# Kernel tuning notes

Hardware: AMD Instinct MI355X
Metric: run time of the kernel (lower is better)

The kernel has to match this reference:

```python
import jax, jax.numpy as jnp
import numpy as np
import math

EMBED = 256
HEADS = 8
HD = EMBED // HEADS  # 32
NB = 3               # n_behaviors
C = NB * NB + 1      # 10 behavior-pair classes
NUM_BUCKETS = 32
MAX_DIST = 40
EPS = 1e-12
B, L = 4, 512


def _rel_bucket(seq_len, num_buckets=NUM_BUCKETS, max_distance=MAX_DIST):
    """T5-style relative position buckets, matching RelativePositionBias._relative_position_bucket."""
    pos = jnp.arange(seq_len)
    relative_position = pos[None, :] - pos[:, None]  # k - q
    n = -relative_position
    nb = num_buckets // 2
    ret = (n < 0).astype(jnp.int32) * nb
    n = jnp.abs(n)
    max_exact = nb // 2
    is_small = n < max_exact
    nf = jnp.maximum(n, 1).astype(jnp.float32)  # clamp to avoid log(0); masked by is_small anyway
    val_large = max_exact + (jnp.log(nf / max_exact) / math.log(max_distance / max_exact) * (nb - max_exact)).astype(jnp.int32)
    val_large = jnp.minimum(val_large, nb - 1)
    return ret + jnp.where(is_small, n, val_large)


def setup_inputs() -> dict:
    key = jax.random.key(0)
    ks = jax.random.split(key, 12)
    s = 0.02
    return {
        "input_tensor": jax.random.normal(ks[0], (B, L, EMBED), jnp.float32),
        "attention_mask": jnp.zeros((B, 1, L, L), jnp.float32),
        "type_seq": jax.random.randint(ks[1], (B, L), 0, NB + 1),
        "Wq": jax.random.normal(ks[2], (NB + 1, EMBED, HEADS, HD), jnp.float32) * s,
        "Wk": jax.random.normal(ks[3], (NB + 1, EMBED, HEADS, HD), jnp.float32) * s,
        "Wv": jax.random.normal(ks[4], (NB + 1, EMBED, HEADS, HD), jnp.float32) * s,
        "W1": jax.random.normal(ks[5], (NB, HEADS, HD, HD), jnp.float32) * s,
        "alpha1": jax.random.normal(ks[6], (C, NB, HEADS), jnp.float32),
        "W2": jax.random.normal(ks[7], (NB, HEADS, HD, HD), jnp.float32) * s,
        "alpha2": jax.random.normal(ks[8], (C, NB, HEADS), jnp.float32),
        "rp_tables": jax.random.normal(ks[9], (C, NUM_BUCKETS, HEADS), jnp.float32) * s,
        "ln_gamma": jnp.ones((EMBED,), jnp.float32),
        "ln_beta": jnp.zeros((EMBED,), jnp.float32),
    }


def reference(input_tensor, attention_mask, type_seq, Wq, Wk, Wv, W1, alpha1, W2, alpha2, rp_tables, ln_gamma, ln_beta):
    bsz, seq_len, emb = input_tensor.shape
    ts = type_seq
    # behavior pair matrix: 0 if either side is padding, else (tq-1)*NB + tk in [1, NB^2]
    bm = ((ts[:, :, None] * ts[:, None, :]) != 0).astype(jnp.int32)
    bm = bm * ((ts[:, :, None] - 1) * NB + ts[:, None, :])  # [B,L,L]

    # --- relative position bias, gathered per behavior pair ---
    bucket = _rel_bucket(seq_len)                 # [L,L]
    vals = rp_tables[:, bucket, :]                # [C,L,L,H]
    qi = jnp.arange(seq_len)[None, :, None]
    ki = jnp.arange(seq_len)[None, None, :]
    bias = vals[bm, qi, ki]                       # [B,L,L,H] gathered along C per pair
    bias = jnp.transpose(bias, (0, 3, 1, 2))      # [B,H,L,L]

    # --- behavior-gated QKV ---
    oh = jax.nn.one_hot(ts, NB + 1, dtype=input_tensor.dtype)  # [B,L,NB+1]
    q = jnp.einsum('BLH,bHhd,BLb->BhLd', input_tensor, Wq, oh)
    k = jnp.einsum('BLH,bHhd,BLb->BhLd', input_tensor, Wk, oh)
    v = jnp.einsum('BLH,bHhd,BLb->BhLd', input_tensor, Wv, oh)

    # --- bilinear scores with per-pair mixing matrices ---
    W1_ = jnp.einsum('bhmn,Cbh->Chmn', W1, jax.nn.softmax(alpha1, axis=1))
    att_all = jnp.einsum('BhQm,Chmn,BhKn->BhQKC', q, W1_, k)  # [B,H,L,L,C]
    scores = jnp.take_along_axis(att_all, bm[:, None, :, :, None], axis=4)[..., 0]
    scores = scores * (1.0 / math.sqrt(HD)) + bias + attention_mask
    probs = jax.nn.softmax(scores, axis=-1)  # dropout=0.0 -> identity

    # --- behavior-mixed value aggregation ---
    W2_ = jnp.einsum('bhmn,Cbh->Chmn', W2, jax.nn.softmax(alpha2, axis=1))
    oh_bm = jax.nn.one_hot(bm, C, dtype=probs.dtype)          # [B,L,L,C]
    pC = probs[:, :, :, :, None] * oh_bm[:, None]             # [B,H,L,L,C]
    ctx = jnp.einsum('BhQKC,Chnm,BhKn->BhQm', pC, W2_, v)     # [B,H,L,d]

    ctx = jnp.transpose(ctx, (0, 2, 1, 3)).reshape(bsz, seq_len, emb)
    x = ctx + input_tensor  # out_dropout=0.0
    mu = jnp.mean(x, axis=-1, keepdims=True)
    var = jnp.mean(jnp.square(x - mu), axis=-1, keepdims=True)
    return (x - mu) / jnp.sqrt(var + EPS) * ln_gamma + ln_beta
```

## Files before the change

### kernel.cpp

```cpp
#include <hip/hip_runtime.h>
#include <math.h>

#define BB 4
#define LL 512
#define EMB 256
#define NH 8
#define HD 32
#define NB_ 3
#define CCN 10
#define NBKT 32
#define SCALE 0.17677669529663687f

typedef __bf16 bf16_t;
typedef __attribute__((ext_vector_type(8))) bf16_t bf16x8;
typedef __attribute__((ext_vector_type(4))) float f32x4;

__device__ __forceinline__ unsigned short f2b(float f) {
    unsigned int u = __float_as_uint(f);
    u += 0x7FFF + ((u >> 16) & 1);
    return (unsigned short)(u >> 16);
}
__device__ __forceinline__ float b2f(unsigned short s) {
    return __uint_as_float(((unsigned int)s) << 16);
}
__device__ __forceinline__ unsigned pack2(float a, float b) {
    return (unsigned)f2b(a) | ((unsigned)f2b(b) << 16);
}
__device__ __forceinline__ int bm_of(int tq, int tk) {
    return (tq * tk != 0) ? ((tq - 1) * 3 + tk) : 0;
}
__device__ __forceinline__ unsigned long long shfl_up64(unsigned long long v, int d) {
    unsigned lo = (unsigned)__shfl_up((int)(unsigned)v, d, 64);
    unsigned hi = (unsigned)__shfl_up((int)(v >> 32), d, 64);
    return (((unsigned long long)hi) << 32) | lo;
}

__device__ __forceinline__ void sort512(const int* __restrict__ tsb, int* spk,
                                        unsigned long long* wtll, int* msc, int tid) {
    int ty0 = tsb[2 * tid], ty1 = tsb[2 * tid + 1];
    unsigned long long pk = (1ULL << (16 * ty0)) + (1ULL << (16 * ty1));
    unsigned long long v = pk;
    int lane = tid & 63;
#pragma unroll
    for (int off = 1; off < 64; off <<= 1) {
        unsigned long long o = shfl_up64(v, off);
        if (lane >= off) v += o;
    }
    int w = tid >> 6;
    if (lane == 63) wtll[w] = v;
    __syncthreads();
    unsigned long long pre = 0, tot = 0;
#pragma unroll
    for (int i = 0; i < 4; i++) {
        unsigned long long xx = wtll[i];
        if (i < w) pre += xx;
        tot += xx;
    }
    v += pre;
    unsigned long long excl = v - pk;
    int c0 = (int)(tot & 0xFFFF), c1 = (int)((tot >> 16) & 0xFFFF);
    int c2 = (int)((tot >> 32) & 0xFFFF), c3 = (int)((tot >> 48) & 0xFFFF);
    int ub0 = 0, ub1 = c0, ub2 = c0 + c1, ub3 = c0 + c1 + c2;
    if (tid == 0) {
        int pc0 = (c0 + 31) & ~31, pc1 = (c1 + 31) & ~31, pc2 = (c2 + 31) & ~31, pc3 = (c3 + 31) & ~31;
        int pb1 = pc0, pb2 = pc0 + pc1, pb3 = pc0 + pc1 + pc2;
        msc[0] = 0;  msc[1] = pb1; msc[2] = pb2; msc[3] = pb3;
        msc[4] = ub0; msc[5] = ub1; msc[6] = ub2; msc[7] = ub3;
        msc[8] = c0; msc[9] = c1; msc[10] = c2; msc[11] = c3;
        msc[12] = (pb3 + pc3 + 63) & ~63;
    }
    int bases[4] = {ub0, ub1, ub2, ub3};
    int r0 = (int)((excl >> (16 * ty0)) & 0xFFFF);
    unsigned long long excl1 = excl + (1ULL << (16 * ty0));
    int r1 = (int)((excl1 >> (16 * ty1)) & 0xFFFF);
    spk[bases[ty0] + r0] = (ty0 << 16) | (2 * tid);
    spk[bases[ty1] + r1] = (ty1 << 16) | (2 * tid + 1);
    __syncthreads();
}

__device__ __forceinline__ void pad_lookup(const int* msc, int pos, int& real, int& upos, int& seg) {
    seg = (pos >= msc[1]) + (pos >= msc[2]) + (pos >= msc[3]);
    int r = pos - msc[seg];
    real = (r < msc[8 + seg]) ? 1 : 0;
    upos = msc[4 + seg] + r;
}

__global__ void k_pre(const float* __restrict__ Wq, const float* __restrict__ Wk, const float* __restrict__ Wv,
                      const int* __restrict__ ts, unsigned short* __restrict__ Wt,
                      int* __restrict__ spkg, int* __restrict__ mscg, int* __restrict__ kpadg,
                      short* __restrict__ tblg, int* __restrict__ cntg) {
    __shared__ unsigned short ls[64 * 264];
    __shared__ int spk_s[LL];
    __shared__ unsigned long long wtll[4];
    __shared__ int msc_s[16];
    int g = blockIdx.x, tid = threadIdx.x;
    if (g < 48) {
        int t = g;
        int tw = t >> 2, ob = t & 3;
        int which = tw >> 2, ty = tw & 3;
        const float* src = ((which == 0) ? Wq : (which == 1) ? Wk : Wv) + (size_t)ty * EMB * EMB;
        int out0 = ob * 64;
        for (int it = 0; it < 16; it++) {
            int e = it * 16 + (tid >> 4);
            int o4 = (tid & 15) * 4;
            float4 v = *(const float4*)&src[(size_t)e * EMB + out0 + o4];
            ls[(o4 + 0) * 264 + e] = f2b(v.x);
            ls[(o4 + 1) * 264 + e] = f2b(v.y);
            ls[(o4 + 2) * 264 + e] = f2b(v.z);
            ls[(o4 + 3) * 264 + e] = f2b(v.w);
        }
        __syncthreads();
        int out = tid >> 2, ech = (tid & 3) * 8;
        unsigned short* dst = Wt + (size_t)tw * EMB * EMB + (size_t)(out0 + out) * EMB;
        const unsigned short* srcl = &ls[out * 264];
#pragma unroll
        for (int jj = 0; jj < 8; jj++)
            *(uint4*)&dst[ech + jj * 32] = *(const uint4*)&srcl[ech + jj * 32];
        return;
    }
    if (g == 48) {
        for (int d = tid; d < LL; d += 256) {
            int v;
            if (d < 8) v = d;
            else {
                double r = log((double)d / 8.0) / log(5.0);
                v = 8 + (int)(r * 8.0);
                if (v > 15) v = 15;
            }
            tblg[d] = (short)v;
        }
        if (tid == 0) cntg[128] = 0;
        return;
    }
    {
        int b = g - 49;
        sort512(ts + b * LL, spk_s, wtll, msc_s, tid);
        for (int i = tid; i < LL; i += 256) spkg[b * LL + i] = spk_s[i];
        if (tid < 16) mscg[b * 16 + tid] = msc_s[tid];
        int KT = msc_s[12];
        for (int pos = tid; pos < KT; pos += 256) {
            int real, upos, seg;
            pad_lookup(msc_s, pos, real, upos, seg);
            int orig = real ? (spk_s[upos] & 0xFFFF) : 0x3FF;
            kpadg[b * 640 + pos] = (seg << 20) | ((real ? upos : 0) << 10) | orig;
        }
    }
}

__global__ __launch_bounds__(256, 4) void k_qkv(
    const float* __restrict__ x, const int* __restrict__ spkg, const int* __restrict__ mscg,
    const unsigned short* __restrict__ Wt,
    const float* __restrict__ A1, const float* __restrict__ W1,
    const float* __restrict__ A2, const float* __restrict__ W2,
    const float* __restrict__ am,
    float* __restrict__ W1s, float* __restrict__ W2s,
    unsigned short* __restrict__ W1Tb, unsigned short* __restrict__ W2Tb,
    int* __restrict__ cntg,
    unsigned short* __restrict__ qp, unsigned short* __restrict__ kp,
    unsigned short* __restrict__ vpT) {
    __shared__ int spk[LL];
    __shared__ int msc[16];
    __shared__ __align__(16) unsigned short vt_l[128 * 33];

    int g = blockIdx.x, tid = threadIdx.x;

    if (g >= 384) {
        int gg = g - 384;
        if (gg < 160) {
            float* cmbf = (float*)vt_l;
            int idx = gg;
            const float* alpha = (idx < 80) ? A1 : A2;
            const float* W     = (idx < 80) ? W1 : W2;
            float* Ws          = (idx < 80) ? W1s : W2s;
            unsigned short* WT = (idx < 80) ? W1Tb : W2Tb;
            idx %= 80;
            int cc = idx / NH, h = idx % NH;
            float a0 = alpha[cc * NB_ * NH + 0 * NH + h];
            float a1 = alpha[cc * NB_ * NH + 1 * NH + h];
            float a2 = alpha[cc * NB_ * NH + 2 * NH + h];
            float mx = fmaxf(a0, fmaxf(a1, a2));
            float e0 = __expf(a0 - mx), e1 = __expf(a1 - mx), e2 = __expf(a2 - mx);
            float inv = 1.0f / (e0 + e1 + e2);
            e0 *= inv; e1 *= inv; e2 *= inv;
            for (int i = tid; i < HD * HD; i += 256) {
                int m = i >> 5, n = i & 31;
                float acc = e0 * W[((0 * NH + h) * HD + m) * HD + n]
                          + e1 * W[((1 * NH + h) * HD + m) * HD + n]
                          + e2 * W[((2 * NH + h) * HD + m) * HD + n];
                cmbf[m * 33 + n] = acc;
            }
            __syncthreads();
            for (int i = tid; i < HD * HD; i += 256) {
                int a = i >> 5, bq = i & 31;
                Ws[((cc * NH + h) * HD + a) * HD + bq] = cmbf[a * 33 + bq];
                WT[((size_t)(cc * NH + h) * HD + a) * HD + bq] = f2b(cmbf[bq * 33 + a]);
            }
        } else {
            int idx = gg - 160;
            const uint4* p = (const uint4*)am + (size_t)idx * 1024;
            unsigned o = 0;
#pragma unroll
            for (int j = 0; j < 4; j++) {
                uint4 v = p[tid + j * 256];
                o |= v.x | v.y | v.z | v.w;
            }
            int wv = __any(o != 0);
            if ((tid & 63) == 0 && wv) atomicOr(&cntg[128], 1);
        }
        return;
    }

    int ns = g % 6, gb = g / 6;
    int b = gb >> 4, tb = gb & 15, i0 = tb * 32;
    int which = ns >> 1, nh = ns & 1;
    int wave = tid >> 6, lane = tid & 63, quad = lane >> 4, col = lane & 15;

    spk[tid] = spkg[b * LL + tid];
    spk[tid + 256] = spkg[b * LL + tid + 256];
    if (tid < 16) msc[tid] = mscg[b * 16 + tid];
    __syncthreads();

    bf16x8 afr[2][8];
#pragma unroll
    for (int mt = 0; mt < 2; mt++) {
        int orig = spk[i0 + mt * 16 + col] & 0xFFFF;
        const float* xr = &x[(size_t)(b * LL + orig) * EMB];
#pragma unroll
        for (int kc = 0; kc < 8; kc++) {
            float4 v0 = *(const float4*)&xr[kc * 32 + quad * 8];
            float4 v1 = *(const float4*)&xr[kc * 32 + quad * 8 + 4];
            uint4 up;
            up.x = pack2(v0.x, v0.y); up.y = pack2(v0.z, v0.w);
            up.z = pack2(v1.x, v1.y); up.w = pack2(v1.z, v1.w);
            afr[mt][kc] = *(bf16x8*)&up;
        }
    }
    int t_start = spk[i0] >> 16, t_end = spk[i0 + 31] >> 16;
    unsigned short* outp = (which == 0) ? qp : kp;

    for (int ty = t_start; ty <= t_end; ty++) {
        f32x4 acc[2][2];
#pragma unroll
        for (int mt = 0; mt < 2; mt++)
#pragma unroll
            for (int nt = 0; nt < 2; nt++) acc[mt][nt] = (f32x4){0.f, 0.f, 0.f, 0.f};
        const unsigned short* wsrc = Wt + (size_t)(which * 4 + ty) * EMB * EMB + (size_t)(nh * 128) * EMB;
        const unsigned short* w0 = &wsrc[(size_t)((wave * 2 + 0) * 16 + col) * EMB + quad * 8];
        const unsigned short* w1 = &wsrc[(size_t)((wave * 2 + 1) * 16 + col) * EMB + quad * 8];
#pragma unroll
        for (int kc = 0; kc < 8; kc++) {
            bf16x8 b0 = *(const bf16x8*)&w0[kc * 32];
            bf16x8 b1 = *(const bf16x8*)&w1[kc * 32];
            acc[0][0] = __builtin_amdgcn_mfma_f32_16x16x32_bf16(afr[0][kc], b0, acc[0][0], 0, 0, 0);
            acc[0][1] = __builtin_amdgcn_mfma_f32_16x16x32_bf16(afr[0][kc], b1, acc[0][1], 0, 0, 0);
            acc[1][0] = __builtin_amdgcn_mfma_f32_16x16x32_bf16(afr[1][kc], b0, acc[1][0], 0, 0, 0);
            acc[1][1] = __builtin_amdgcn_mfma_f32_16x16x32_bf16(afr[1][kc], b1, acc[1][1], 0, 0, 0);
        }
        if (which < 2) {
#pragma unroll
            for (int mt = 0; mt < 2; mt++)
#pragma unroll
                for (int r = 0; r < 4; r++) {
                    int tokloc = mt * 16 + quad * 4 + r;
                    int tty = spk[i0 + tokloc] >> 16;
                    if (tty != ty) continue;
#pragma unroll
                    for (int nt = 0; nt < 2; nt++) {
                        int n = nh * 128 + (wave * 2 + nt) * 16 + col;
                        int h = n >> 5, d = n & 31;
                        outp[((size_t)(b * NH + h) * LL + i0 + tokloc) * HD + d] = f2b(acc[mt][nt][r]);
                    }
                }
        } else {
#pragma unroll
            for (int mt = 0; mt < 2; mt++)
#pragma unroll
                for (int nt = 0; nt < 2; nt++) {
                    int ln = (wave * 2 + nt) * 16 + col;
#pragma unroll
                    for (int r = 0; r < 4; r++)
                        vt_l[ln * 33 + mt * 16 + quad * 4 + r] = f2b(acc[mt][nt][r]);
                }
            __syncthreads();
            int ub = msc[4 + ty], cnt = msc[8 + ty], pb = msc[ty];
            int lo = ub - i0; if (lo < 0) lo = 0;
            int hi = ub + cnt - i0; if (hi > 32) hi = 32;
            int run = hi - lo;
            int pbase = pb + i0 + lo - ub;
            int rowbase = b * 256 + nh * 128;
            int t32 = tid & 31;
            if (t32 < run) {
                for (int rr = tid >> 5; rr < 128; rr += 8)
                    vpT[(size_t)(rowbase + rr) * 640 + pbase + t32] = vt_l[rr * 33 + lo + t32];
            }
            __syncthreads();
        }
    }
}

#define SCP 648
#define OFF_UN   20736
#define OFF_QTB  29184
#define OFF_KPAD 33536
#define OFF_TBL  36096
#define OFF_RPL  37120
#define OFF_QOR  38400
#define OFF_QTY  38464
#define OFF_INV  38528
#define OFF_PSUM 38592
#define SM_TOTAL 38848
__global__ __launch_bounds__(256, 4) void k_attn(
    const unsigned short* __restrict__ qp, const unsigned short* __restrict__ kp,
    const unsigned short* __restrict__ vpT,
    const int* __restrict__ spkg, const int* __restrict__ mscg, const int* __restrict__ kpadg,
    const short* __restrict__ tblg,
    const float* __restrict__ rp, const float* __restrict__ am,
    const float* __restrict__ W1s, const float* __restrict__ W2s,
    const unsigned short* __restrict__ W1Tb, const unsigned short* __restrict__ W2Tb,
    const int* __restrict__ cntg, float* __restrict__ ctx) {
    __shared__ __align__(16) char smem[SM_TOTAL];
    __shared__ int msk_s;
    unsigned short* scu = (unsigned short*)smem;
    unsigned short* qstb = (unsigned short*)(smem + OFF_UN);
    float* sb   = (float*)(smem + OFF_UN);
    unsigned short* qtb = (unsigned short*)(smem + OFF_QTB);
    unsigned short* sbb = (unsigned short*)(smem + OFF_QTB);
    int*   kpad = (int*)(smem + OFF_KPAD);
    short* tbl  = (short*)(smem + OFF_TBL);
    float* rp_l = (float*)(smem + OFF_RPL);
    int*   qor_l = (int*)(smem + OFF_QOR);
    int*   qty_l = (int*)(smem + OFF_QTY);
    float* inv_l = (float*)(smem + OFF_INV);
    float* psum = (float*)(smem + OFF_PSUM);

    int blk = blockIdx.x;
    int b = blk >> 8, h = (blk >> 5) & 7, q16 = blk & 31;
    int i0q = q16 * 16;
    int tid = threadIdx.x;
    int wave = tid >> 6, lane = tid & 63, quad = lane >> 4, col = lane & 15;
    int bh = b * NH + h;

    int KT = mscg[b * 16 + 12];
    if (tid == 0) msk_s = cntg[128];
    if (tid < 16) {
        int v = spkg[b * LL + i0q + tid];
        qor_l[tid] = v & 0xFFFF; qty_l[tid] = v >> 16;
    }
    if (tid < (KT >> 2)) ((int4*)kpad)[tid] = ((const int4*)(kpadg + b * 640))[tid];
    ((int*)tbl)[tid] = ((const int*)tblg)[tid];
    for (int i = tid; i < CCN * NBKT; i += 256) rp_l[i] = rp[i * NH + h];
    {
        int q = tid >> 4, m2 = (tid & 15) * 2;
        ((unsigned*)qstb)[q * 20 + (tid & 15)] =
            *(const unsigned*)&qp[((size_t)bh * LL + i0q + q) * HD + m2];
    }
    __syncthreads();

    int qor_r[4], qty_r[4];
#pragma unroll
    for (int r = 0; r < 4; r++) { qor_r[r] = qor_l[quad * 4 + r]; qty_r[r] = qty_l[quad * 4 + r]; }
    bool uniq = (qty_l[0] == qty_l[15]);
    int tqu = qty_l[0];
    int tA = qty_l[0], tB = qty_l[15];
    bool two = false;
    if (!uniq) {
        two = true;
#pragma unroll
        for (int i = 0; i < 16; i++) {
            int t = qty_l[i];
            two = two && (t == tA || t == tB);
        }
    }
    int mz = (msk_s == 0);

    if (uniq) {
#pragma unroll
        for (int it = 0; it < 2; it++) {
            int t8 = wave * 2 + it;
            int tk = t8 >> 1, nhf = t8 & 1;
            int bmv = bm_of(tqu, tk);
            bf16x8 a = *(const bf16x8*)&qstb[col * 40 + quad * 8];
            bf16x8 bb = *(const bf16x8*)&W1Tb[((size_t)(bmv * NH + h) * HD + nhf * 16 + col) * HD + quad * 8];
            f32x4 d = {0.f, 0.f, 0.f, 0.f};
            d = __builtin_amdgcn_mfma_f32_16x16x32_bf16(a, bb, d, 0, 0, 0);
#pragma unroll
            for (int r = 0; r < 4; r++)
                qtb[(quad * 4 + r) * 136 + tk * 32 + nhf * 16 + col] = f2b(d[r]);
        }
    } else if (two) {
#pragma unroll
        for (int it = 0; it < 2; it++) {
            int t8 = wave * 2 + it;
            int tk = t8 >> 1, nhf = t8 & 1;
            bf16x8 a = *(const bf16x8*)&qstb[col * 40 + quad * 8];
            bf16x8 bA = *(const bf16x8*)&W1Tb[((size_t)(bm_of(tA, tk) * NH + h) * HD + nhf * 16 + col) * HD + quad * 8];
            bf16x8 bBv = *(const bf16x8*)&W1Tb[((size_t)(bm_of(tB, tk) * NH + h) * HD + nhf * 16 + col) * HD + quad * 8];
            f32x4 dA = {0.f, 0.f, 0.f, 0.f};
            f32x4 dB = {0.f, 0.f, 0.f, 0.f};
            dA = __builtin_amdgcn_mfma_f32_16x16x32_bf16(a, bA, dA, 0, 0, 0);
            dB = __builtin_amdgcn_mfma_f32_16x16x32_bf16(a, bBv, dB, 0, 0, 0);
#pragma unroll
            for (int r = 0; r < 4; r++) {
                float val = (qty_r[r] == tA) ? dA[r] : dB[r];
                qtb[(quad * 4 + r) * 136 + tk * 32 + nhf * 16 + col] = f2b(val);
            }
        }
    } else {
        for (int i = tid; i < 16 * 128; i += 256) {
            int q = i >> 7, r = i & 127, tk = r >> 5, n = r & 31;
            int bmv = bm_of(qty_l[q], tk);
            const float* wb = &W1s[((bmv * NH + h) * HD) * HD + n];
            float acc = 0.f;
#pragma unroll
            for (int m = 0; m < HD; m++) acc += b2f(qstb[q * 40 + m]) * wb[m * HD];
            qtb[q * 136 + tk * 32 + n] = f2b(acc);
        }
    }
    __syncthreads();

    const float* amb = am + (size_t)b * LL * LL;
    int ntiles = KT >> 4;
    if (mz) {
        float rs[4] = {0.f, 0.f, 0.f, 0.f};
        int tqm_r[4], tqz_r[4];
#pragma unroll
        for (int r = 0; r < 4; r++) { tqm_r[r] = (qty_r[r] - 1) * 3; tqz_r[r] = (qty_r[r] != 0); }
        for (int tile = wave; tile < ntiles; tile += 4) {
            int kb = tile * 16;
            int kv0 = kpad[kb];
            if ((kv0 & 0x3FF) == 0x3FF) {
#pragma unroll
                for (int r = 0; r < 4; r++) scu[(quad * 4 + r) * SCP + kb + col] = 0;
                continue;
            }
            int tkt = kv0 >> 20;
            int kpi = kb + col;
            int kv = kpad[kpi];
            int ko = kv & 0x3FF;
            int upos = (kv >> 10) & 0x3FF;
            bool real = (ko != 0x3FF);
            bf16x8 bfr;
            if (real) bfr = *(const bf16x8*)&kp[((size_t)bh * LL + upos) * HD + quad * 8];
            else { uint4 z = make_uint4(0, 0, 0, 0); bfr = *(bf16x8*)&z; }
            bf16x8 a = *(const bf16x8*)&qtb[col * 136 + tkt * 32 + quad * 8];
            f32x4 d = {0.f, 0.f, 0.f, 0.f};
            d = __builtin_amdgcn_mfma_f32_16x16x32_bf16(a, bfr, d, 0, 0, 0);
            if (!real) {
#pragma unroll
                for (int r = 0; r < 4; r++) scu[(quad * 4 + r) * SCP + kpi] = 0;
            } else {
#pragma unroll
                for (int r = 0; r < 4; r++) {
                    int q = quad * 4 + r;
                    int qo = qor_r[r];
                    int dd = qo - ko;
                    int ad = dd < 0 ? -dd : dd;
                    int bk = (dd < 0 ? 16 : 0) + (int)tbl[ad];
                    int bmv = (tqz_r[r] && tkt) ? tqm_r[r] + tkt : 0;
                    float sv = d[r] * SCALE + rp_l[bmv * NBKT + bk];
                    float e = __expf(sv);
                    scu[q * SCP + kpi] = f2b(e);
                    rs[r] += e;
                }
            }
        }
#pragma unroll
        for (int off = 1; off < 16; off <<= 1) {
#pragma unroll
            for (int r = 0; r < 4; r++) rs[r] += __shfl_xor(rs[r], off, 16);
        }
        if (col == 0) {
#pragma unroll
            for (int r = 0; r < 4; r++) psum[wave * 16 + quad * 4 + r] = rs[r];
        }
    } else {
        for (int tile = wave; tile < ntiles; tile += 4) {
            int kb = tile * 16;
            int kv0 = kpad[kb];
            if ((kv0 & 0x3FF) == 0x3FF) {
#pragma unroll
                for (int r = 0; r < 4; r++) scu[(quad * 4 + r) * SCP + kb + col] = 0xFF80;
                continue;
            }
            int tkt = kv0 >> 20;
            int kpi = kb + col;
            int kv = kpad[kpi];
            int ko = kv & 0x3FF;
            int upos = (kv >> 10) & 0x3FF;
            bool real = (ko != 0x3FF);
            bf16x8 bfr;
            if (real) bfr = *(const bf16x8*)&kp[((size_t)bh * LL + upos) * HD + quad * 8];
            else { uint4 z = make_uint4(0, 0, 0, 0); bfr = *(bf16x8*)&z; }
            bf16x8 a = *(const bf16x8*)&qtb[col * 136 + tkt * 32 + quad * 8];
            f32x4 d = {0.f, 0.f, 0.f, 0.f};
            d = __builtin_amdgcn_mfma_f32_16x16x32_bf16(a, bfr, d, 0, 0, 0);
            if (!real) {
#pragma unroll
                for (int r = 0; r < 4; r++) scu[(quad * 4 + r) * SCP + kpi] = 0xFF80;
            } else {
#pragma unroll
                for (int r = 0; r < 4; r++) {
                    int q = quad * 4 + r;
                    int qo = qor_r[r];
                    int dd = qo - ko;
                    int ad = dd < 0 ? -dd : dd;
                    int bk = (dd < 0 ? 16 : 0) + (int)tbl[ad];
                    float sv = d[r] * SCALE + rp_l[bm_of(qty_r[r], tkt) * NBKT + bk];
                    sv += amb[(size_t)qo * LL + ko];
                    scu[q * SCP + kpi] = f2b(sv);
                }
            }
        }
    }
    __syncthreads();

    if (mz) {
        if (tid < 16)
            inv_l[tid] = 1.0f / (psum[tid] + psum[16 + tid] + psum[32 + tid] + psum[48 + tid]);
    } else {
        int gq = tid >> 4, t16 = tid & 15;
        float mx = -1e30f;
        for (int kk = t16; kk < KT; kk += 16) mx = fmaxf(mx, b2f(scu[gq * SCP + kk]));
#pragma unroll
        for (int off = 1; off < 16; off <<= 1) mx = fmaxf(mx, __shfl_xor(mx, off, 16));
        float sum = 0.f;
        for (int kk = t16; kk < KT; kk += 16) {
            int idx = gq * SCP + kk;
            float e = __expf(b2f(scu[idx]) - mx);
            scu[idx] = f2b(e); sum += e;
        }
#pragma unroll
        for (int off = 1; off < 16; off <<= 1) sum += __shfl_xor(sum, off, 16);
        if (t16 == 0) inv_l[gq] = 1.0f / sum;
    }
    __syncthreads();

    const unsigned short* vbase = &vpT[(size_t)(b * 256 + h * 32) * 640];
    f32x4 accv[2];
    accv[0] = (f32x4){0.f, 0.f, 0.f, 0.f};
    accv[1] = (f32x4){0.f, 0.f, 0.f, 0.f};
    {
        int pb = mscg[b * 16 + wave];
        int cnt = mscg[b * 16 + 8 + wave];
        int g0 = pb >> 5, g1 = (pb + cnt + 31) >> 5;
        for (int gg = g0; gg < g1; ++gg) {
            int loc = gg << 5;
            bf16x8 a = *(const bf16x8*)&scu[col * SCP + loc + quad * 8];
            bf16x8 b0 = *(const bf16x8*)&vbase[(size_t)col * 640 + loc + quad * 8];
            bf16x8 b1 = *(const bf16x8*)&vbase[(size_t)(col + 16) * 640 + loc + quad * 8];
            accv[0] = __builtin_amdgcn_mfma_f32_16x16x32_bf16(a, b0, accv[0], 0, 0, 0);
            accv[1] = __builtin_amdgcn_mfma_f32_16x16x32_bf16(a, b1, accv[1], 0, 0, 0);
        }
    }
#pragma unroll
    for (int hh = 0; hh < 2; hh++)
#pragma unroll
        for (int r = 0; r < 4; r++) {
            int q = quad * 4 + r, n = col + 16 * hh;
            float fin = accv[hh][r];
            sb[q * 132 + wave * 32 + n] = fin;
            sbb[q * 136 + wave * 32 + n] = f2b(fin);
        }
    __syncthreads();

    if (uniq) {
        if (wave < 2) {
            int mhf = wave;
            f32x4 d = {0.f, 0.f, 0.f, 0.f};
#pragma unroll
            for (int tk = 0; tk < 4; tk++) {
                int bmv = bm_of(tqu, tk);
                bf16x8 a = *(const bf16x8*)&sbb[col * 136 + tk * 32 + quad * 8];
                bf16x8 bb = *(const bf16x8*)&W2Tb[((size_t)(bmv * NH + h) * HD + mhf * 16 + col) * HD + quad * 8];
                d = __builtin_amdgcn_mfma_f32_16x16x32_bf16(a, bb, d, 0, 0, 0);
            }
#pragma unroll
            for (int r = 0; r < 4; r++) {
                int q = quad * 4 + r;
                ctx[((size_t)(b * LL + qor_l[q])) * EMB + h * HD + mhf * 16 + col] = d[r] * inv_l[q];
            }
        }
    } else if (two) {
        int myT = (wave < 2) ? tA : tB;
        int mhf = wave & 1;
        f32x4 d = {0.f, 0.f, 0.f, 0.f};
#pragma unroll
        for (int tk = 0; tk < 4; tk++) {
            int bmv = bm_of(myT, tk);
            bf16x8 a = *(const bf16x8*)&sbb[col * 136 + tk * 32 + quad * 8];
            bf16x8 bb = *(const bf16x8*)&W2Tb[((size_t)(bmv * NH + h) * HD + mhf * 16 + col) * HD + quad * 8];
            d = __builtin_amdgcn_mfma_f32_16x16x32_bf16(a, bb, d, 0, 0, 0);
        }
#pragma unroll
        for (int r = 0; r < 4; r++) {
            int q = quad * 4 + r;
            if (qty_l[q] == myT)
                ctx[((size_t)(b * LL + qor_l[q])) * EMB + h * HD + mhf * 16 + col] = d[r] * inv_l[q];
        }
    } else {
        int m = tid & 31, qq = tid >> 5;
#pragma unroll
        for (int rep = 0; rep < 2; rep++) {
            int qi = qq + 8 * rep;
            int tq = qty_l[qi];
            float acc = 0.f;
#pragma unroll
            for (int tk2 = 0; tk2 < 4; tk2++) {
                int bmv = bm_of(tq, tk2);
                const float* wb = &W2s[((bmv * NH + h) * HD) * HD + m];
                const float* sbp = &sb[qi * 132 + tk2 * 32];
                for (int n = 0; n < HD; n++) acc += sbp[n] * wb[n * HD];
            }
            int qo = qor_l[qi];
            ctx[((size_t)(b * LL + qo)) * EMB + h * HD + m] = acc * inv_l[qi];
        }
    }
}

__global__ void k_ln(const float* __restrict__ ctx, const float* __restrict__ x,
                     const float* __restrict__ gamma, const float* __restrict__ beta,
                     float* __restrict__ out) {
    int wave = threadIdx.x >> 6, lane = threadIdx.x & 63;
    int tok = blockIdx.x * 4 + wave;
    size_t base = (size_t)tok * EMB + lane * 4;
    float4 c = *(const float4*)&ctx[base];
    float4 xi = *(const float4*)&x[base];
    float4 v;
    v.x = c.x + xi.x; v.y = c.y + xi.y; v.z = c.z + xi.z; v.w = c.w + xi.w;
    float s = v.x + v.y + v.z + v.w;
    float s2 = v.x * v.x + v.y * v.y + v.z * v.z + v.w * v.w;
#pragma unroll
    for (int off = 1; off < 64; off <<= 1) {
        s += __shfl_xor(s, off, 64);
        s2 += __shfl_xor(s2, off, 64);
    }
    float mu = s * (1.0f / EMB);
    float var = s2 * (1.0f / EMB) - mu * mu;
    float r = rsqrtf(var + 1e-12f);
    float4 gg = *(const float4*)&gamma[lane * 4];
    float4 bb = *(const float4*)&beta[lane * 4];
    float4 o;
    o.x = (v.x - mu) * r * gg.x + bb.x;
    o.y = (v.y - mu) * r * gg.y + bb.y;
    o.z = (v.z - mu) * r * gg.z + bb.z;
    o.w = (v.w - mu) * r * gg.w + bb.w;
    *(float4*)&out[base] = o;
}

extern "C" void kernel_launch(void* const* d_in, const int* in_sizes, int n_in,
                              void* d_out, int out_size, void* d_ws, size_t ws_size,
                              hipStream_t stream) {
    const float* x  = (const float*)d_in[0];
    const float* am = (const float*)d_in[1];
    const int*   ts = (const int*)d_in[2];
    const float* Wq = (const float*)d_in[3];
    const float* Wk = (const float*)d_in[4];
    const float* Wv = (const float*)d_in[5];
    const float* W1 = (const float*)d_in[6];
    const float* a1 = (const float*)d_in[7];
    const float* W2 = (const float*)d_in[8];
    const float* a2 = (const float*)d_in[9];
    const float* rp = (const float*)d_in[10];
    const float* g  = (const float*)d_in[11];
    const float* be = (const float*)d_in[12];
    float* out = (float*)d_out;

    float* ws  = (float*)d_ws;
    float* W1s = ws;
    float* W2s = ws + 81920;
    unsigned short* W1Tb = (unsigned short*)(ws + 163840);
    unsigned short* W2Tb = (unsigned short*)(ws + 204800);
    int* cntg = (int*)(ws + 245760);
    int* spkg = (int*)(ws + 246016);
    int* mscg = (int*)(ws + 248064);
    int* kpadg = (int*)(ws + 248128);
    short* tblg = (short*)(ws + 250688);
    unsigned short* qp = (unsigned short*)(ws + 250944);
    unsigned short* kp = qp + BB * NH * LL * HD;
    unsigned short* vpT = kp + BB * NH * LL * HD;
    float* ctx = (float*)(vpT + BB * 256 * 640);
    unsigned short* Wt = (unsigned short*)ctx;

    hipLaunchKernelGGL(k_pre, dim3(53), dim3(256), 0, stream,
                       Wq, Wk, Wv, ts, Wt, spkg, mscg, kpadg, tblg, cntg);
    hipLaunchKernelGGL(k_qkv, dim3(800), dim3(256), 0, stream,
                       x, spkg, mscg, Wt, a1, W1, a2, W2, am, W1s, W2s, W1Tb, W2Tb, cntg,
                       qp, kp, vpT);
    hipLaunchKernelGGL(k_attn, dim3(BB * NH * 32), dim3(256), 0, stream,
                       qp, kp, vpT, spkg, mscg, kpadg, tblg, rp, am, W1s, W2s, W1Tb, W2Tb,
                       cntg, ctx);
    hipLaunchKernelGGL(k_ln, dim3(BB * LL / 4), dim3(256), 0, stream, ctx, x, g, be, out);
}
```

Before: 124.3 us.

## Fuse preprocessing kernel into QKV projection kernel and drop weight pre-transpose

New measurement: 118.9 us. 4.4% less time.

```diff
diff --git a/kernel.cpp b/kernel.cpp
--- a/kernel.cpp
+++ b/kernel.cpp
@@ -85,80 +85,21 @@
     upos = msc[4 + seg] + r;
 }
 
-__global__ void k_pre(const float* __restrict__ Wq, const float* __restrict__ Wk, const float* __restrict__ Wv,
-                      const int* __restrict__ ts, unsigned short* __restrict__ Wt,
-                      int* __restrict__ spkg, int* __restrict__ mscg, int* __restrict__ kpadg,
-                      short* __restrict__ tblg, int* __restrict__ cntg) {
-    __shared__ unsigned short ls[64 * 264];
-    __shared__ int spk_s[LL];
-    __shared__ unsigned long long wtll[4];
-    __shared__ int msc_s[16];
-    int g = blockIdx.x, tid = threadIdx.x;
-    if (g < 48) {
-        int t = g;
-        int tw = t >> 2, ob = t & 3;
-        int which = tw >> 2, ty = tw & 3;
-        const float* src = ((which == 0) ? Wq : (which == 1) ? Wk : Wv) + (size_t)ty * EMB * EMB;
-        int out0 = ob * 64;
-        for (int it = 0; it < 16; it++) {
-            int e = it * 16 + (tid >> 4);
-            int o4 = (tid & 15) * 4;
-            float4 v = *(const float4*)&src[(size_t)e * EMB + out0 + o4];
-            ls[(o4 + 0) * 264 + e] = f2b(v.x);
-            ls[(o4 + 1) * 264 + e] = f2b(v.y);
-            ls[(o4 + 2) * 264 + e] = f2b(v.z);
-            ls[(o4 + 3) * 264 + e] = f2b(v.w);
-        }
-        __syncthreads();
-        int out = tid >> 2, ech = (tid & 3) * 8;
-        unsigned short* dst = Wt + (size_t)tw * EMB * EMB + (size_t)(out0 + out) * EMB;
-        const unsigned short* srcl = &ls[out * 264];
-#pragma unroll
-        for (int jj = 0; jj < 8; jj++)
-            *(uint4*)&dst[ech + jj * 32] = *(const uint4*)&srcl[ech + jj * 32];
-        return;
-    }
-    if (g == 48) {
-        for (int d = tid; d < LL; d += 256) {
-            int v;
-            if (d < 8) v = d;
-            else {
-                double r = log((double)d / 8.0) / log(5.0);
-                v = 8 + (int)(r * 8.0);
-                if (v > 15) v = 15;
-            }
-            tblg[d] = (short)v;
-        }
-        if (tid == 0) cntg[128] = 0;
-        return;
-    }
-    {
-        int b = g - 49;
-        sort512(ts + b * LL, spk_s, wtll, msc_s, tid);
-        for (int i = tid; i < LL; i += 256) spkg[b * LL + i] = spk_s[i];
-        if (tid < 16) mscg[b * 16 + tid] = msc_s[tid];
-        int KT = msc_s[12];
-        for (int pos = tid; pos < KT; pos += 256) {
-            int real, upos, seg;
-            pad_lookup(msc_s, pos, real, upos, seg);
-            int orig = real ? (spk_s[upos] & 0xFFFF) : 0x3FF;
-            kpadg[b * 640 + pos] = (seg << 20) | ((real ? upos : 0) << 10) | orig;
-        }
-    }
-}
-
-__global__ __launch_bounds__(256, 4) void k_qkv(
-    const float* __restrict__ x, const int* __restrict__ spkg, const int* __restrict__ mscg,
-    const unsigned short* __restrict__ Wt,
+__global__ __launch_bounds__(256, 4) void k_main(
+    const float* __restrict__ x, const int* __restrict__ ts,
+    const float* __restrict__ Wq, const float* __restrict__ Wk, const float* __restrict__ Wv,
     const float* __restrict__ A1, const float* __restrict__ W1,
     const float* __restrict__ A2, const float* __restrict__ W2,
     const float* __restrict__ am,
     float* __restrict__ W1s, float* __restrict__ W2s,
     unsigned short* __restrict__ W1Tb, unsigned short* __restrict__ W2Tb,
-    int* __restrict__ cntg,
+    int* __restrict__ mfl,
+    int* __restrict__ spkg, int* __restrict__ mscg, int* __restrict__ kpadg,
+    short* __restrict__ tblg,
     unsigned short* __restrict__ qp, unsigned short* __restrict__ kp,
     unsigned short* __restrict__ vpT) {
     __shared__ int spk[LL];
+    __shared__ unsigned long long wtll[4];
     __shared__ int msc[16];
     __shared__ __align__(16) unsigned short vt_l[128 * 33];
 
@@ -195,17 +136,47 @@
                 Ws[((cc * NH + h) * HD + a) * HD + bq] = cmbf[a * 33 + bq];
                 WT[((size_t)(cc * NH + h) * HD + a) * HD + bq] = f2b(cmbf[bq * 33 + a]);
             }
-        } else {
+            return;
+        }
+        if (gg < 288) {
+            int* reds = (int*)wtll;
             int idx = gg - 160;
-            const uint4* p = (const uint4*)am + (size_t)idx * 1024;
+            const uint4* p = (const uint4*)am + (size_t)idx * 2048;
             unsigned o = 0;
 #pragma unroll
-            for (int j = 0; j < 4; j++) {
+            for (int j = 0; j < 8; j++) {
                 uint4 v = p[tid + j * 256];
                 o |= v.x | v.y | v.z | v.w;
             }
             int wv = __any(o != 0);
-            if ((tid & 63) == 0 && wv) atomicOr(&cntg[128], 1);
+            if ((tid & 63) == 0) reds[tid >> 6] = wv;
+            __syncthreads();
+            if (tid == 0) mfl[idx] = reds[0] | reds[1] | reds[2] | reds[3];
+            return;
+        }
+        if (gg < 292) {
+            int b = gg - 288;
+            sort512(ts + b * LL, spk, wtll, msc, tid);
+            for (int i = tid; i < LL; i += 256) spkg[b * LL + i] = spk[i];
+            if (tid < 16) mscg[b * 16 + tid] = msc[tid];
+            int KT = msc[12];
+            for (int pos = tid; pos < KT; pos += 256) {
+                int real, upos, seg;
+                pad_lookup(msc, pos, real, upos, seg);
+                int orig = real ? (spk[upos] & 0xFFFF) : 0x3FF;
+                kpadg[b * 640 + pos] = (seg << 20) | ((real ? upos : 0) << 10) | orig;
+            }
+            return;
+        }
+        for (int d = tid; d < LL; d += 256) {
+            int v;
+            if (d < 8) v = d;
+            else {
+                double r = log((double)d / 8.0) / log(5.0);
+                v = 8 + (int)(r * 8.0);
+                if (v > 15) v = 15;
+            }
+            tblg[d] = (short)v;
         }
         return;
     }
@@ -215,10 +186,7 @@
     int which = ns >> 1, nh = ns & 1;
     int wave = tid >> 6, lane = tid & 63, quad = lane >> 4, col = lane & 15;
 
-    spk[tid] = spkg[b * LL + tid];
-    spk[tid + 256] = spkg[b * LL + tid + 256];
-    if (tid < 16) msc[tid] = mscg[b * 16 + tid];
-    __syncthreads();
+    sort512(ts + b * LL, spk, wtll, msc, tid);
 
     bf16x8 afr[2][8];
 #pragma unroll
@@ -237,20 +205,33 @@
     }
     int t_start = spk[i0] >> 16, t_end = spk[i0 + 31] >> 16;
     unsigned short* outp = (which == 0) ? qp : kp;
+    const float* wmat = (which == 0) ? Wq : (which == 1) ? Wk : Wv;
+
+    int n_0 = nh * 128 + (wave * 2 + 0) * 16 + col;
 
     for (int ty = t_start; ty <= t_end; ty++) {
+        const float* wty = wmat + (size_t)ty * EMB * EMB;
+        const float* wc0 = wty + (size_t)(quad * 8) * EMB + n_0;
+        const float* wc1 = wc0 + 16;
         f32x4 acc[2][2];
 #pragma unroll
         for (int mt = 0; mt < 2; mt++)
 #pragma unroll
             for (int nt = 0; nt < 2; nt++) acc[mt][nt] = (f32x4){0.f, 0.f, 0.f, 0.f};
-        const unsigned short* wsrc = Wt + (size_t)(which * 4 + ty) * EMB * EMB + (size_t)(nh * 128) * EMB;
-        const unsigned short* w0 = &wsrc[(size_t)((wave * 2 + 0) * 16 + col) * EMB + quad * 8];
-        const unsigned short* w1 = &wsrc[(size_t)((wave * 2 + 1) * 16 + col) * EMB + quad * 8];
 #pragma unroll
         for (int kc = 0; kc < 8; kc++) {
-            bf16x8 b0 = *(const bf16x8*)&w0[kc * 32];
-            bf16x8 b1 = *(const bf16x8*)&w1[kc * 32];
+            const float* p0 = wc0 + (size_t)kc * 32 * EMB;
+            const float* p1 = wc1 + (size_t)kc * 32 * EMB;
+            float f0[8], f1[8];
+#pragma unroll
+            for (int j = 0; j < 8; j++) { f0[j] = p0[j * EMB]; f1[j] = p1[j * EMB]; }
+            uint4 u0, u1;
+            u0.x = pack2(f0[0], f0[1]); u0.y = pack2(f0[2], f0[3]);
+            u0.z = pack2(f0[4], f0[5]); u0.w = pack2(f0[6], f0[7]);
+            u1.x = pack2(f1[0], f1[1]); u1.y = pack2(f1[2], f1[3]);
+            u1.z = pack2(f1[4], f1[5]); u1.w = pack2(f1[6], f1[7]);
+            bf16x8 b0 = *(bf16x8*)&u0;
+            bf16x8 b1 = *(bf16x8*)&u1;
             acc[0][0] = __builtin_amdgcn_mfma_f32_16x16x32_bf16(afr[0][kc], b0, acc[0][0], 0, 0, 0);
             acc[0][1] = __builtin_amdgcn_mfma_f32_16x16x32_bf16(afr[0][kc], b1, acc[0][1], 0, 0, 0);
             acc[1][0] = __builtin_amdgcn_mfma_f32_16x16x32_bf16(afr[1][kc], b0, acc[1][0], 0, 0, 0);
@@ -266,7 +247,7 @@
                     if (tty != ty) continue;
 #pragma unroll
                     for (int nt = 0; nt < 2; nt++) {
-                        int n = nh * 128 + (wave * 2 + nt) * 16 + col;
+                        int n = n_0 + nt * 16;
                         int h = n >> 5, d = n & 31;
                         outp[((size_t)(b * NH + h) * LL + i0 + tokloc) * HD + d] = f2b(acc[mt][nt][r]);
                     }
@@ -317,7 +298,7 @@
     const float* __restrict__ rp, const float* __restrict__ am,
     const float* __restrict__ W1s, const float* __restrict__ W2s,
     const unsigned short* __restrict__ W1Tb, const unsigned short* __restrict__ W2Tb,
-    const int* __restrict__ cntg, float* __restrict__ ctx) {
+    const int* __restrict__ mfl, float* __restrict__ ctx) {
     __shared__ __align__(16) char smem[SM_TOTAL];
     __shared__ int msk_s;
     unsigned short* scu = (unsigned short*)smem;
@@ -341,7 +322,11 @@
     int bh = b * NH + h;
 
     int KT = mscg[b * 16 + 12];
-    if (tid == 0) msk_s = cntg[128];
+    if (wave == 0) {
+        int v = mfl[lane] | mfl[64 + lane];
+        int anyv = __any(v != 0);
+        if (lane == 0) msk_s = anyv;
+    }
     if (tid < 16) {
         int v = spkg[b * LL + i0q + tid];
         qor_l[tid] = v & 0xFFFF; qty_l[tid] = v >> 16;
@@ -670,7 +655,7 @@
     float* W2s = ws + 81920;
     unsigned short* W1Tb = (unsigned short*)(ws + 163840);
     unsigned short* W2Tb = (unsigned short*)(ws + 204800);
-    int* cntg = (int*)(ws + 245760);
+    int* mfl  = (int*)(ws + 245760);
     int* spkg = (int*)(ws + 246016);
     int* mscg = (int*)(ws + 248064);
     int* kpadg = (int*)(ws + 248128);
@@ -679,15 +664,13 @@
     unsigned short* kp = qp + BB * NH * LL * HD;
     unsigned short* vpT = kp + BB * NH * LL * HD;
     float* ctx = (float*)(vpT + BB * 256 * 640);
-    unsigned short* Wt = (unsigned short*)ctx;
-
-    hipLaunchKernelGGL(k_pre, dim3(53), dim3(256), 0, stream,
-                       Wq, Wk, Wv, ts, Wt, spkg, mscg, kpadg, tblg, cntg);
-    hipLaunchKernelGGL(k_qkv, dim3(800), dim3(256), 0, stream,
-                       x, spkg, mscg, Wt, a1, W1, a2, W2, am, W1s, W2s, W1Tb, W2Tb, cntg,
+
+    hipLaunchKernelGGL(k_main, dim3(677), dim3(256), 0, stream,
+                       x, ts, Wq, Wk, Wv, a1, W1, a2, W2, am,
+                       W1s, W2s, W1Tb, W2Tb, mfl, spkg, mscg, kpadg, tblg,
                        qp, kp, vpT);
     hipLaunchKernelGGL(k_attn, dim3(BB * NH * 32), dim3(256), 0, stream,
                        qp, kp, vpT, spkg, mscg, kpadg, tblg, rp, am, W1s, W2s, W1Tb, W2Tb,
-                       cntg, ctx);
+                       mfl, ctx);
     hipLaunchKernelGGL(k_ln, dim3(BB * LL / 4), dim3(256), 0, stream, ctx, x, g, be, out);
 }
```
